# Performance work log

Hardware: AMD Instinct MI355X
Metric: run time of the kernel (lower is better)

## Reference

```python
import jax, jax.numpy as jnp
import numpy as np

B, S, D = 2, 2048, 2048
H = 16
Q_LORA = 1024
KV_LORA = 512
NOPE = 128
ROPE = 64
VH = 128
QK = NOPE + ROPE
EPS = 1e-3
SCALE = QK ** -0.5


def rms_norm(x, w):
    x32 = x.astype(jnp.float32)
    n = x32 * jax.lax.rsqrt(jnp.mean(x32 * x32, axis=-1, keepdims=True) + EPS)
    return w * n.astype(x.dtype)


def apply_rope(x, cos, sin):
    # x: [b, s, h, d]; cos/sin: [1, s, 1, d//2].
    # torch view_as_complex pairs consecutive elements: (x0,x1),(x2,x3),...
    xr, xi = x[..., 0::2], x[..., 1::2]
    yr = xr * cos - xi * sin
    yi = xr * sin + xi * cos
    return jnp.stack([yr, yi], axis=-1).reshape(x.shape)


def setup_inputs() -> dict:
    key = jax.random.key(0)
    ks = jax.random.split(key, 8)

    def lin(k, out, inn):
        bound = 1.0 / float(np.sqrt(inn))
        return jax.random.uniform(k, (out, inn), jnp.float32, -bound, bound)

    inv_freq = 1.0 / (10000.0 ** (np.arange(0, ROPE, 2, dtype=np.float32) / ROPE))
    ang = np.arange(S, dtype=np.float32)[:, None] * inv_freq[None, :]  # [S, ROPE/2]
    return {
        "x": jax.random.normal(ks[0], (B, S, D), jnp.float32),
        "start_pos": 0,
        "cos": jnp.asarray(np.cos(ang), jnp.float32),
        "sin": jnp.asarray(np.sin(ang), jnp.float32),
        "wq_a_w": lin(ks[1], Q_LORA, D),
        "wq_a_b": jnp.zeros((Q_LORA,), jnp.float32),
        "q_norm_w": jnp.ones((Q_LORA,), jnp.float32),
        "wq_b_w": lin(ks[2], H * QK, Q_LORA),
        "wq_b_b": jnp.zeros((H * QK,), jnp.float32),
        "wkv_a_w": lin(ks[3], KV_LORA + ROPE, D),
        "wkv_a_b": jnp.zeros((KV_LORA + ROPE,), jnp.float32),
        "kv_norm_w": jnp.ones((KV_LORA,), jnp.float32),
        "wkv_b_w": lin(ks[4], H * (NOPE + VH), KV_LORA),
        "wo_w": lin(ks[5], D, H * VH),
        "wo_b": jnp.zeros((D,), jnp.float32),
    }


def reference(x, start_pos, cos, sin, wq_a_w, wq_a_b, q_norm_w, wq_b_w, wq_b_b,
              wkv_a_w, wkv_a_b, kv_norm_w, wkv_b_w, wo_w, wo_b):
    b, s, _ = x.shape
    cos_ = cos[None, :, None, :]
    sin_ = sin[None, :, None, :]

    # q path: low-rank down-proj, RMSNorm, up-proj
    q = rms_norm(x @ wq_a_w.T + wq_a_b, q_norm_w) @ wq_b_w.T + wq_b_b
    q = q.reshape(b, s, H, QK)
    q_nope, q_pe = q[..., :NOPE], q[..., NOPE:]
    q_pe = apply_rope(q_pe, cos_, sin_)

    # kv path: joint low-rank latent + rope key
    kv_full = x @ wkv_a_w.T + wkv_a_b
    kv, k_pe = kv_full[..., :KV_LORA], kv_full[..., KV_LORA:]
    k_pe = apply_rope(k_pe[:, :, None, :], cos_, sin_)[:, :, 0, :]  # [b, t, ROPE]

    wkv_b = wkv_b_w.reshape(H, NOPE + VH, KV_LORA)
    # absorb k up-projection into q (MLA trick): q_nope -> latent space
    q_nope = jnp.einsum('bshd,hdc->bshc', q_nope, wkv_b[:, :NOPE])  # [b,s,H,KV_LORA]

    kv_c = rms_norm(kv, kv_norm_w)  # latent KV cache contents [b, t, KV_LORA]

    scores = (jnp.einsum('bshc,btc->bsht', q_nope, kv_c)
              + jnp.einsum('bshr,btr->bsht', q_pe, k_pe)) * SCALE
    # NOTE: source builds a causal mask but never adds it -> plain softmax (faithful)
    probs = jax.nn.softmax(scores.astype(jnp.float32), axis=-1).astype(x.dtype)

    o = jnp.einsum('bsht,btc->bshc', probs, kv_c)          # latent output
    o = jnp.einsum('bshc,hdc->bshd', o, wkv_b[:, NOPE:])    # v up-projection
    return o.reshape(b, s, H * VH) @ wo_w.T + wo_b
```

## Files before the change

### kernel.cpp

```cpp
#include <hip/hip_runtime.h>
#include <stdint.h>

typedef uint16_t u16;
typedef __bf16 bf16x8 __attribute__((ext_vector_type(8)));
typedef float f32x4 __attribute__((ext_vector_type(4)));

#define EPS 1e-3f
#define SCALE_F 0.07216878364870323f

__device__ __forceinline__ float bf2f(u16 u) {
    union { uint32_t i; float f; } v; v.i = ((uint32_t)u) << 16; return v.f;
}
__device__ __forceinline__ u16 f2bf(float f) {
    union { float f; uint32_t i; } v; v.f = f;
    uint32_t x = v.i;
    return (u16)((x + 0x7fffu + ((x >> 16) & 1u)) >> 16);
}

__device__ __forceinline__ void async_cp16(const u16* g, u16* l) {
    __builtin_amdgcn_global_load_lds(
        (const __attribute__((address_space(1))) uint32_t*)g,
        (__attribute__((address_space(3))) uint32_t*)l,
        16, 0, 0);
}

struct Cvt {
    const void* src[14];
    u16* dst[14];
    long off[15];
};

__global__ __launch_bounds__(256) void cvt_kernel(Cvt c, const uint32_t* qnw_u32, long total8)
{
    const long i8 = (long)blockIdx.x * 256 + threadIdx.x;
    if (i8 >= total8) return;
    const long e = i8 * 8;
    const bool is_f32 = (qnw_u32[0] == 0x3F800000u);
    int t = 0;
    while (e >= c.off[t + 1]) ++t;
    const long local = e - c.off[t];
    u16* d = c.dst[t] + local;
    if (is_f32) {
        const float* s = (const float*)c.src[t] + local;
        #pragma unroll
        for (int j = 0; j < 8; ++j) d[j] = f2bf(s[j]);
    } else {
        const u16* s = (const u16*)c.src[t] + local;
        #pragma unroll
        for (int j = 0; j < 8; ++j) d[j] = s[j];
    }
}

__global__ __launch_bounds__(256) void gemm_bt_kernel(
    const u16* __restrict__ A, const u16* __restrict__ B,
    const u16* __restrict__ bias, u16* __restrict__ C,
    int M, int N, int K, int lda, int ldb, int ldc, float alpha, int c_f32,
    int z0, int hcnt,
    long sAl, long sAb, long sAh,
    long sBl, long sBb, long sBh,
    long sCl, long sCb, long sCh)
{
    const int zl = blockIdx.z;
    const int zg = z0 + zl;
    const int zb = zg / hcnt, zh = zg - zb * hcnt;
    A += (long)zl * sAl + (long)zb * sAb + (long)zh * sAh;
    B += (long)zl * sBl + (long)zb * sBb + (long)zh * sBh;
    C += (long)zl * sCl + (long)zb * sCb + (long)zh * sCh;

    __shared__ u16 As[128 * 32];
    __shared__ u16 Bs[128 * 32];

    const int tid  = threadIdx.x;
    const int wave = tid >> 6, lane = tid & 63;
    const int wm = (wave >> 1) << 6, wn = (wave & 1) << 6;
    const int quad = lane >> 4, r15 = lane & 15;

    const int tileM = blockIdx.y * 128;
    const int tileN = blockIdx.x * 128;

    const int c0 = tid, c1 = tid + 256;
    const int rA0 = c0 >> 2, kb0 = (c0 & 3) << 3;
    const int rA1 = c1 >> 2, kb1 = (c1 & 3) << 3;
    int rB0 = tileN + rA0; if (rB0 > N - 1) rB0 = N - 1;
    int rB1 = tileN + rA1; if (rB1 > N - 1) rB1 = N - 1;

    const u16* Ag0 = A + (long)(tileM + rA0) * lda + kb0;
    const u16* Ag1 = A + (long)(tileM + rA1) * lda + kb1;
    const u16* Bg0 = B + (long)rB0 * ldb + kb0;
    const u16* Bg1 = B + (long)rB1 * ldb + kb1;
    u16* lA0 = &As[c0 << 3];
    u16* lA1 = &As[c1 << 3];
    u16* lB0 = &Bs[c0 << 3];
    u16* lB1 = &Bs[c1 << 3];

    f32x4 acc[4][4] = {};

    const u16* aRd[4]; const u16* bRd[4];
    #pragma unroll
    for (int i = 0; i < 4; ++i) {
        aRd[i] = &As[(wm + i * 16 + r15) * 32 + quad * 8];
        bRd[i] = &Bs[(wn + i * 16 + r15) * 32 + quad * 8];
    }

    for (int k0 = 0; k0 < K; k0 += 32) {
        async_cp16(Ag0, lA0);
        async_cp16(Ag1, lA1);
        async_cp16(Bg0, lB0);
        async_cp16(Bg1, lB1);
        Ag0 += 32; Ag1 += 32; Bg0 += 32; Bg1 += 32;
        __syncthreads();
        bf16x8 af[4], bfr[4];
        #pragma unroll
        for (int i = 0; i < 4; ++i) {
            af[i]  = *(const bf16x8*)aRd[i];
            bfr[i] = *(const bf16x8*)bRd[i];
        }
        #pragma unroll
        for (int mi = 0; mi < 4; ++mi)
            #pragma unroll
            for (int ni = 0; ni < 4; ++ni)
                acc[mi][ni] = __builtin_amdgcn_mfma_f32_16x16x32_bf16(
                    af[mi], bfr[ni], acc[mi][ni], 0, 0, 0);
        __syncthreads();
    }

    #pragma unroll
    for (int mi = 0; mi < 4; ++mi) {
        const int row = tileM + wm + mi * 16 + quad * 4;
        #pragma unroll
        for (int ni = 0; ni < 4; ++ni) {
            const int col = tileN + wn + ni * 16 + r15;
            if (col < N) {
                if (c_f32) {
                    const float bv = bias ? bf2f(bias[col]) : 0.f;
                    #pragma unroll
                    for (int r = 0; r < 4; ++r)
                        ((float*)C)[(long)(row + r) * ldc + col] =
                            acc[mi][ni][r] * alpha + bv;
                } else {
                    #pragma unroll
                    for (int r = 0; r < 4; ++r) {
                        u16 t = f2bf(acc[mi][ni][r] * alpha);
                        if (bias) t = f2bf(bf2f(t) + bf2f(bias[col]));
                        C[(long)(row + r) * ldc + col] = t;
                    }
                }
            }
        }
    }
}

#define PS 72

__global__ __launch_bounds__(256, 2) void flash_kernel(
    const u16* __restrict__ q, const u16* __restrict__ K2,
    const u16* __restrict__ Vt, u16* __restrict__ O)
{
    __shared__ __align__(16) u16 Ks[64 * 192];
    __shared__ __align__(16) u16 Vs[128 * 64];
    __shared__ __align__(16) u16 Ps[4][32 * PS];

    const int bid = blockIdx.x;
    const int xcd = bid & 7;
    const int idx = bid >> 3;
    const int bh  = xcd * 4 + (idx >> 4);
    const int mt  = idx & 15;
    const int b = bh >> 4, h = bh & 15;

    const int tid = threadIdx.x;
    const int wave = tid >> 6, lane = tid & 63;
    const int quad = lane >> 4, r15 = lane & 15;
    const int r7 = r15 & 7;

    const long qrow0 = (long)b * 2048 + mt * 128 + wave * 32;
    u16* myPs = Ps[wave];

    bf16x8 qf[2][6];
    #pragma unroll
    for (int mi = 0; mi < 2; ++mi) {
        const u16* qp = q + (qrow0 + mi * 16 + r15) * 3072 + h * 192 + quad * 8;
        #pragma unroll
        for (int kst = 0; kst < 6; ++kst)
            qf[mi][kst] = *(const bf16x8*)(qp + kst * 32);
    }

    f32x4 Oacc[2][8] = {};
    float m_i[2][4], l_i[2][4];
    #pragma unroll
    for (int mi = 0; mi < 2; ++mi)
        #pragma unroll
        for (int r = 0; r < 4; ++r) { m_i[mi][r] = -1e30f; l_i[mi][r] = 0.f; }

    const u16* Kbh = K2 + (long)b * 2048 * 3072 + h * 192;
    const u16* Vbh = Vt + (long)bh * 128 * 2048;

    const u16* gK[6];
    #pragma unroll
    for (int i = 0; i < 6; ++i) {
        const int c = i * 256 + tid;
        const int row = c / 24, s = c - row * 24;
        gK[i] = Kbh + (long)row * 3072 + ((s ^ (row & 7)) << 3);
    }
    const u16* gV[4];
    #pragma unroll
    for (int i = 0; i < 4; ++i) {
        const int c = i * 256 + tid;
        const int d = c >> 3, s = c & 7;
        gV[i] = Vbh + (long)d * 2048 + ((s ^ (d & 7)) << 3);
    }

    #pragma unroll
    for (int i = 0; i < 6; ++i) {
        async_cp16(gK[i], &Ks[(i * 256 + tid) << 3]);
        gK[i] += 64 * 3072;
    }
    __syncthreads();

    for (int j = 0; j < 32; ++j) {
        #pragma unroll
        for (int i = 0; i < 4; ++i) {
            async_cp16(gV[i], &Vs[(i * 256 + tid) << 3]);
            gV[i] += 64;
        }

        f32x4 S[2][4] = {};
        #pragma unroll
        for (int kst = 0; kst < 6; ++kst) {
            bf16x8 bfr[4];
            #pragma unroll
            for (int ni = 0; ni < 4; ++ni)
                bfr[ni] = *(const bf16x8*)&Ks[(ni * 16 + r15) * 192
                                              + (((kst * 4 + quad) ^ r7) << 3)];
            #pragma unroll
            for (int mi = 0; mi < 2; ++mi)
                #pragma unroll
                for (int ni = 0; ni < 4; ++ni)
                    S[mi][ni] = __builtin_amdgcn_mfma_f32_16x16x32_bf16(
                        qf[mi][kst], bfr[ni], S[mi][ni], 0, 0, 0);
        }
        #pragma unroll
        for (int mi = 0; mi < 2; ++mi)
            #pragma unroll
            for (int ni = 0; ni < 4; ++ni)
                #pragma unroll
                for (int r = 0; r < 4; ++r)
                    S[mi][ni][r] *= SCALE_F;

        __syncthreads();

        #pragma unroll
        for (int i = 0; i < 6; ++i) {
            async_cp16(gK[i], &Ks[(i * 256 + tid) << 3]);
            gK[i] += 64 * 3072;
        }

        #pragma unroll
        for (int mi = 0; mi < 2; ++mi)
            #pragma unroll
            for (int r = 0; r < 4; ++r) {
                float t = S[mi][0][r];
                #pragma unroll
                for (int ni = 1; ni < 4; ++ni) t = fmaxf(t, S[mi][ni][r]);
                t = fmaxf(t, __shfl_xor(t, 1, 16));
                t = fmaxf(t, __shfl_xor(t, 2, 16));
                t = fmaxf(t, __shfl_xor(t, 4, 16));
                t = fmaxf(t, __shfl_xor(t, 8, 16));
                const float mnew = fmaxf(m_i[mi][r], t);
                const float al = __expf(m_i[mi][r] - mnew);
                m_i[mi][r] = mnew;
                const int lrow = mi * 16 + quad * 4 + r;
                float ps = 0.f;
                #pragma unroll
                for (int ni = 0; ni < 4; ++ni) {
                    const float pv = __expf(S[mi][ni][r] - mnew);
                    ps += pv;
                    myPs[lrow * PS + ni * 16 + r15] = f2bf(pv);
                }
                #pragma unroll
                for (int ni = 0; ni < 8; ++ni) Oacc[mi][ni][r] *= al;
                ps += __shfl_xor(ps, 1, 16);
                ps += __shfl_xor(ps, 2, 16);
                ps += __shfl_xor(ps, 4, 16);
                ps += __shfl_xor(ps, 8, 16);
                l_i[mi][r] = l_i[mi][r] * al + ps;
            }

        #pragma unroll
        for (int kst = 0; kst < 2; ++kst) {
            bf16x8 af[2], bv[8];
            #pragma unroll
            for (int mi = 0; mi < 2; ++mi)
                af[mi] = *(const bf16x8*)&myPs[(mi * 16 + r15) * PS
                                               + kst * 32 + quad * 8];
            #pragma unroll
            for (int ni = 0; ni < 8; ++ni)
                bv[ni] = *(const bf16x8*)&Vs[(ni * 16 + r15) * 64
                                             + (((kst * 4 + quad) ^ r7) << 3)];
            #pragma unroll
            for (int mi = 0; mi < 2; ++mi)
                #pragma unroll
                for (int ni = 0; ni < 8; ++ni)
                    Oacc[mi][ni] = __builtin_amdgcn_mfma_f32_16x16x32_bf16(
                        af[mi], bv[ni], Oacc[mi][ni], 0, 0, 0);
        }

        __syncthreads();
    }

    #pragma unroll
    for (int mi = 0; mi < 2; ++mi)
        #pragma unroll
        for (int r = 0; r < 4; ++r) {
            const float inv = 1.f / l_i[mi][r];
            const long row = qrow0 + mi * 16 + quad * 4 + r;
            #pragma unroll
            for (int ni = 0; ni < 8; ++ni)
                O[row * 2048 + h * 128 + ni * 16 + r15] =
                    f2bf(Oacc[mi][ni][r] * inv);
        }
}

__global__ __launch_bounds__(256) void rmsnorm_kernel(
    const u16* __restrict__ x, const u16* __restrict__ w, u16* __restrict__ y, int n)
{
    const long row = blockIdx.x;
    const u16* xr = x + row * n;
    u16* yr = y + row * n;
    const int tid = threadIdx.x;
    const int cnt = n >> 8;
    float v[4];
    float ss = 0.f;
    for (int i = 0; i < cnt; ++i) { v[i] = bf2f(xr[tid + (i << 8)]); ss += v[i] * v[i]; }
    for (int o = 32; o; o >>= 1) ss += __shfl_xor(ss, o, 64);
    __shared__ float sm[4];
    if ((tid & 63) == 0) sm[tid >> 6] = ss;
    __syncthreads();
    const float rinv = rsqrtf((sm[0] + sm[1] + sm[2] + sm[3]) / (float)n + EPS);
    for (int i = 0; i < cnt; ++i) {
        const u16 nb = f2bf(v[i] * rinv);
        yr[tid + (i << 8)] = f2bf(bf2f(w[tid + (i << 8)]) * bf2f(nb));
    }
}

__global__ __launch_bounds__(256) void kv_kernel(
    const u16* __restrict__ cosb, const u16* __restrict__ sinb,
    const u16* __restrict__ w, u16* __restrict__ kvf)
{
    const long bs = blockIdx.x;
    const int s = (int)(bs & 2047);
    u16* io = kvf + bs * 576;
    const int tid = threadIdx.x;
    const float v0 = bf2f(io[tid * 2]), v1 = bf2f(io[tid * 2 + 1]);
    float ss = v0 * v0 + v1 * v1;
    for (int off = 32; off; off >>= 1) ss += __shfl_xor(ss, off, 64);
    __shared__ float sm[4];
    if ((tid & 63) == 0) sm[tid >> 6] = ss;
    __syncthreads();
    const float rinv = rsqrtf((sm[0] + sm[1] + sm[2] + sm[3]) / 512.f + EPS);
    const u16 n0 = f2bf(v0 * rinv), n1 = f2bf(v1 * rinv);
    io[tid * 2]     = f2bf(bf2f(w[tid * 2]) * bf2f(n0));
    io[tid * 2 + 1] = f2bf(bf2f(w[tid * 2 + 1]) * bf2f(n1));
    if (tid < 32) {
        const int j = tid;
        const float xr = bf2f(io[512 + 2 * j]), xi = bf2f(io[512 + 2 * j + 1]);
        const float c = bf2f(cosb[s * 32 + j]), si = bf2f(sinb[s * 32 + j]);
        io[512 + 2 * j]     = f2bf(bf2f(f2bf(xr * c))  - bf2f(f2bf(xi * si)));
        io[512 + 2 * j + 1] = f2bf(bf2f(f2bf(xr * si)) + bf2f(f2bf(xi * c)));
    }
}

__global__ __launch_bounds__(256) void rope_q_kernel(
    const u16* __restrict__ cosb, const u16* __restrict__ sinb, u16* __restrict__ q)
{
    const int idx = blockIdx.x * 256 + threadIdx.x;
    const int j = idx & 31;
    const int h = (idx >> 5) & 15;
    const int bs = idx >> 9;
    const int s = bs & 2047;
    u16* p = q + (long)bs * 3072 + h * 192 + 128 + 2 * j;
    const float xr = bf2f(p[0]), xi = bf2f(p[1]);
    const float c = bf2f(cosb[s * 32 + j]), si = bf2f(sinb[s * 32 + j]);
    p[0] = f2bf(bf2f(f2bf(xr * c))  - bf2f(f2bf(xi * si)));
    p[1] = f2bf(bf2f(f2bf(xr * si)) + bf2f(f2bf(xi * c)));
}

__global__ __launch_bounds__(256) void k2rope_kernel(
    const u16* __restrict__ kvf, u16* __restrict__ K2)
{
    const long row = blockIdx.x;
    const int tid = threadIdx.x;
    #pragma unroll
    for (int i = 0; i < 4; ++i) {
        const int slot = tid + (i << 8);
        const int h = slot >> 6, r = slot & 63;
        K2[row * 3072 + h * 192 + 128 + r] = kvf[row * 576 + 512 + r];
    }
}

extern "C" void kernel_launch(void* const* d_in, const int* in_sizes, int n_in,
                              void* d_out, int out_size, void* d_ws, size_t ws_size,
                              hipStream_t stream)
{
    float* out = (float*)d_out;

    char* p = (char*)d_ws;
    auto alloc = [&](size_t elems) { u16* r = (u16*)p; p += elems * 2; return r; };
    u16* c_cos  = alloc(65536);
    u16* c_sin  = alloc(65536);
    u16* c_wqa  = alloc(2097152);
    u16* c_wqab = alloc(1024);
    u16* c_qnw  = alloc(1024);
    u16* c_wqb  = alloc(3145728);
    u16* c_wqbb = alloc(3072);
    u16* c_wkva = alloc(1179648);
    u16* c_wkvab= alloc(576);
    u16* c_kvnw = alloc(512);
    u16* c_wkvb = alloc(2097152);
    u16* c_wo   = alloc(4194304);
    u16* c_wob  = alloc(2048);
    u16* q   = alloc(4096UL * 3072);
    u16* kvf = alloc(4096UL * 576);
    u16* K2  = alloc(4096UL * 3072);
    u16* O   = alloc(4096UL * 2048);
    u16* q_a = (u16*)p;
    u16* xb = (u16*)d_out;
    u16* Vt = (u16*)d_out + 8388608;

    Cvt cv;
    const long sizes[14] = {8388608, 65536, 65536, 2097152, 1024, 1024, 3145728,
                            3072, 1179648, 576, 512, 2097152, 4194304, 2048};
    u16* dsts[14] = {xb, c_cos, c_sin, c_wqa, c_wqab, c_qnw, c_wqb, c_wqbb,
                     c_wkva, c_wkvab, c_kvnw, c_wkvb, c_wo, c_wob};
    const int srcidx[14] = {0, 2, 3, 4, 5, 6, 7, 8, 9, 10, 11, 12, 13, 14};
    long acc_off = 0;
    for (int t = 0; t < 14; ++t) {
        cv.src[t] = d_in[srcidx[t]];
        cv.dst[t] = dsts[t];
        cv.off[t] = acc_off;
        acc_off += sizes[t];
    }
    cv.off[14] = acc_off;
    const long total8 = acc_off / 8;
    cvt_kernel<<<dim3((unsigned)((total8 + 255) / 256)), dim3(256), 0, stream>>>(
        cv, (const uint32_t*)d_in[6], total8);

    auto gemm = [&](const u16* A, const u16* B, const u16* bias, u16* C,
                    int M, int N, int K, int lda, int ldb, int ldc, float alpha,
                    int c_f32, int nz, int z0, int hcnt,
                    long sAl, long sAb, long sAh,
                    long sBl, long sBb, long sBh,
                    long sCl, long sCb, long sCh) {
        dim3 grid((N + 127) / 128, M / 128, nz);
        gemm_bt_kernel<<<grid, dim3(256), 0, stream>>>(
            A, B, bias, C, M, N, K, lda, ldb, ldc, alpha, c_f32, z0, hcnt,
            sAl, sAb, sAh, sBl, sBb, sBh, sCl, sCb, sCh);
    };

    gemm(xb, c_wqa, c_wqab, q_a, 4096, 1024, 2048, 2048, 2048, 1024, 1.f, 0,
         1, 0, 1, 0, 0, 0, 0, 0, 0, 0, 0, 0);
    rmsnorm_kernel<<<4096, 256, 0, stream>>>(q_a, c_qnw, q_a, 1024);
    gemm(q_a, c_wqb, c_wqbb, q, 4096, 3072, 1024, 1024, 1024, 3072, 1.f, 0,
         1, 0, 1, 0, 0, 0, 0, 0, 0, 0, 0, 0);
    gemm(xb, c_wkva, c_wkvab, kvf, 4096, 576, 2048, 2048, 2048, 576, 1.f, 0,
         1, 0, 1, 0, 0, 0, 0, 0, 0, 0, 0, 0);
    kv_kernel<<<4096, 256, 0, stream>>>(c_cos, c_sin, c_kvnw, kvf);
    rope_q_kernel<<<8192, 256, 0, stream>>>(c_cos, c_sin, q);
    gemm(kvf, c_wkvb, nullptr, K2, 4096, 128, 512, 576, 512, 3072, 1.f, 0,
         16, 0, 16, 0, 0, 0, 0, 0, 256L * 512, 0, 0, 192);
    k2rope_kernel<<<4096, 256, 0, stream>>>(kvf, K2);
    gemm(c_wkvb + 128 * 512, kvf, nullptr, Vt, 128, 2048, 512, 512, 576, 2048, 1.f, 0,
         32, 0, 16,
         0, 0, 256L * 512,
         0, 2048L * 576, 0,
         0, 16L * 128 * 2048, 128L * 2048);
    flash_kernel<<<dim3(512), dim3(256), 0, stream>>>(q, K2, Vt, O);
    gemm(O, c_wo, c_wob, (u16*)out, 4096, 2048, 2048, 2048, 2048, 2048, 1.f, 1,
         1, 0, 1, 0, 0, 0, 0, 0, 0, 0, 0, 0);
}
```

Measured before the change: 579.4 us.

## Deepen GEMM K-tile, lazy softmax rescale, fold scale into exp, add setprio

The GEMM kernel now stages a K-tile of 64 instead of 32 in shared memory, halving the number of barrier pairs per K loop at the cost of double the LDS footprint. The attention kernel drops the separate scaling pass and folds SCALE into the exp argument. It also skips the running-max update and the O/l rescale whenever every row's new max stays within a threshold of the old one. MFMA sections are wrapped in s_setprio to favour matrix issue across waves. The lazy rescale relies on the fixed threshold keeping exp values within fp32/bf16 range.

```diff
diff --git a/kernel.cpp b/kernel.cpp
--- a/kernel.cpp
+++ b/kernel.cpp
@@ -7,6 +7,7 @@
 
 #define EPS 1e-3f
 #define SCALE_F 0.07216878364870323f
+#define THR_RAW 110.0f
 
 __device__ __forceinline__ float bf2f(u16 u) {
     union { uint32_t i; float f; } v; v.i = ((uint32_t)u) << 16; return v.f;
@@ -67,8 +68,8 @@
     B += (long)zl * sBl + (long)zb * sBb + (long)zh * sBh;
     C += (long)zl * sCl + (long)zb * sCb + (long)zh * sCh;
 
-    __shared__ u16 As[128 * 32];
-    __shared__ u16 Bs[128 * 32];
+    __shared__ u16 As[128 * 64];
+    __shared__ u16 Bs[128 * 64];
 
     const int tid  = threadIdx.x;
     const int wave = tid >> 6, lane = tid & 63;
@@ -78,49 +79,51 @@
     const int tileM = blockIdx.y * 128;
     const int tileN = blockIdx.x * 128;
 
-    const int c0 = tid, c1 = tid + 256;
-    const int rA0 = c0 >> 2, kb0 = (c0 & 3) << 3;
-    const int rA1 = c1 >> 2, kb1 = (c1 & 3) << 3;
-    int rB0 = tileN + rA0; if (rB0 > N - 1) rB0 = N - 1;
-    int rB1 = tileN + rA1; if (rB1 > N - 1) rB1 = N - 1;
-
-    const u16* Ag0 = A + (long)(tileM + rA0) * lda + kb0;
-    const u16* Ag1 = A + (long)(tileM + rA1) * lda + kb1;
-    const u16* Bg0 = B + (long)rB0 * ldb + kb0;
-    const u16* Bg1 = B + (long)rB1 * ldb + kb1;
-    u16* lA0 = &As[c0 << 3];
-    u16* lA1 = &As[c1 << 3];
-    u16* lB0 = &Bs[c0 << 3];
-    u16* lB1 = &Bs[c1 << 3];
+    const u16* Ag[4]; const u16* Bg[4];
+    u16* lA[4]; u16* lB[4];
+    #pragma unroll
+    for (int i = 0; i < 4; ++i) {
+        const int cc = i * 256 + tid;
+        const int rA = cc >> 3, kb = (cc & 7) << 3;
+        int rB = tileN + rA; if (rB > N - 1) rB = N - 1;
+        Ag[i] = A + (long)(tileM + rA) * lda + kb;
+        Bg[i] = B + (long)rB * ldb + kb;
+        lA[i] = &As[cc << 3];
+        lB[i] = &Bs[cc << 3];
+    }
 
     f32x4 acc[4][4] = {};
 
     const u16* aRd[4]; const u16* bRd[4];
     #pragma unroll
     for (int i = 0; i < 4; ++i) {
-        aRd[i] = &As[(wm + i * 16 + r15) * 32 + quad * 8];
-        bRd[i] = &Bs[(wn + i * 16 + r15) * 32 + quad * 8];
-    }
-
-    for (int k0 = 0; k0 < K; k0 += 32) {
-        async_cp16(Ag0, lA0);
-        async_cp16(Ag1, lA1);
-        async_cp16(Bg0, lB0);
-        async_cp16(Bg1, lB1);
-        Ag0 += 32; Ag1 += 32; Bg0 += 32; Bg1 += 32;
+        aRd[i] = &As[(wm + i * 16 + r15) * 64 + quad * 8];
+        bRd[i] = &Bs[(wn + i * 16 + r15) * 64 + quad * 8];
+    }
+
+    for (int k0 = 0; k0 < K; k0 += 64) {
+        #pragma unroll
+        for (int i = 0; i < 4; ++i) {
+            async_cp16(Ag[i], lA[i]);
+            async_cp16(Bg[i], lB[i]);
+            Ag[i] += 64; Bg[i] += 64;
+        }
         __syncthreads();
-        bf16x8 af[4], bfr[4];
-        #pragma unroll
-        for (int i = 0; i < 4; ++i) {
-            af[i]  = *(const bf16x8*)aRd[i];
-            bfr[i] = *(const bf16x8*)bRd[i];
-        }
-        #pragma unroll
-        for (int mi = 0; mi < 4; ++mi)
-            #pragma unroll
-            for (int ni = 0; ni < 4; ++ni)
-                acc[mi][ni] = __builtin_amdgcn_mfma_f32_16x16x32_bf16(
-                    af[mi], bfr[ni], acc[mi][ni], 0, 0, 0);
+        #pragma unroll
+        for (int kk = 0; kk < 2; ++kk) {
+            bf16x8 af[4], bfr[4];
+            #pragma unroll
+            for (int i = 0; i < 4; ++i) {
+                af[i]  = *(const bf16x8*)(aRd[i] + kk * 32);
+                bfr[i] = *(const bf16x8*)(bRd[i] + kk * 32);
+            }
+            #pragma unroll
+            for (int mi = 0; mi < 4; ++mi)
+                #pragma unroll
+                for (int ni = 0; ni < 4; ++ni)
+                    acc[mi][ni] = __builtin_amdgcn_mfma_f32_16x16x32_bf16(
+                        af[mi], bfr[ni], acc[mi][ni], 0, 0, 0);
+        }
         __syncthreads();
     }
 
@@ -224,6 +227,7 @@
         }
 
         f32x4 S[2][4] = {};
+        __builtin_amdgcn_s_setprio(1);
         #pragma unroll
         for (int kst = 0; kst < 6; ++kst) {
             bf16x8 bfr[4];
@@ -238,13 +242,7 @@
                     S[mi][ni] = __builtin_amdgcn_mfma_f32_16x16x32_bf16(
                         qf[mi][kst], bfr[ni], S[mi][ni], 0, 0, 0);
         }
-        #pragma unroll
-        for (int mi = 0; mi < 2; ++mi)
-            #pragma unroll
-            for (int ni = 0; ni < 4; ++ni)
-                #pragma unroll
-                for (int r = 0; r < 4; ++r)
-                    S[mi][ni][r] *= SCALE_F;
+        __builtin_amdgcn_s_setprio(0);
 
         __syncthreads();
 
@@ -254,6 +252,8 @@
             gK[i] += 64 * 3072;
         }
 
+        float tmax[2][4];
+        float gmax = -1e30f;
         #pragma unroll
         for (int mi = 0; mi < 2; ++mi)
             #pragma unroll
@@ -265,26 +265,43 @@
                 t = fmaxf(t, __shfl_xor(t, 2, 16));
                 t = fmaxf(t, __shfl_xor(t, 4, 16));
                 t = fmaxf(t, __shfl_xor(t, 8, 16));
-                const float mnew = fmaxf(m_i[mi][r], t);
-                const float al = __expf(m_i[mi][r] - mnew);
-                m_i[mi][r] = mnew;
+                tmax[mi][r] = t;
+                gmax = fmaxf(gmax, t - m_i[mi][r]);
+            }
+        if (!__all(gmax <= THR_RAW)) {
+            #pragma unroll
+            for (int mi = 0; mi < 2; ++mi)
+                #pragma unroll
+                for (int r = 0; r < 4; ++r) {
+                    const float mnew = fmaxf(m_i[mi][r], tmax[mi][r]);
+                    const float al = __expf((m_i[mi][r] - mnew) * SCALE_F);
+                    m_i[mi][r] = mnew;
+                    l_i[mi][r] *= al;
+                    #pragma unroll
+                    for (int ni = 0; ni < 8; ++ni) Oacc[mi][ni][r] *= al;
+                }
+        }
+        #pragma unroll
+        for (int mi = 0; mi < 2; ++mi)
+            #pragma unroll
+            for (int r = 0; r < 4; ++r) {
                 const int lrow = mi * 16 + quad * 4 + r;
+                const float mm = m_i[mi][r];
                 float ps = 0.f;
                 #pragma unroll
                 for (int ni = 0; ni < 4; ++ni) {
-                    const float pv = __expf(S[mi][ni][r] - mnew);
+                    const float pv = __expf((S[mi][ni][r] - mm) * SCALE_F);
                     ps += pv;
                     myPs[lrow * PS + ni * 16 + r15] = f2bf(pv);
                 }
-                #pragma unroll
-                for (int ni = 0; ni < 8; ++ni) Oacc[mi][ni][r] *= al;
                 ps += __shfl_xor(ps, 1, 16);
                 ps += __shfl_xor(ps, 2, 16);
                 ps += __shfl_xor(ps, 4, 16);
                 ps += __shfl_xor(ps, 8, 16);
-                l_i[mi][r] = l_i[mi][r] * al + ps;
+                l_i[mi][r] += ps;
             }
 
+        __builtin_amdgcn_s_setprio(1);
         #pragma unroll
         for (int kst = 0; kst < 2; ++kst) {
             bf16x8 af[2], bv[8];
@@ -303,6 +320,7 @@
                     Oacc[mi][ni] = __builtin_amdgcn_mfma_f32_16x16x32_bf16(
                         af[mi], bv[ni], Oacc[mi][ni], 0, 0, 0);
         }
+        __builtin_amdgcn_s_setprio(0);
 
         __syncthreads();
     }
```

Measured after the change: 574.4 us. About the same (-0.9%).
